# Optimization experiments

Measured on AMD Instinct MI355X. Metric: run time of the kernel, lower is better.

The kernel has to match this reference:

```python
import jax, jax.numpy as jnp
import numpy as np

KEY_IN = 256
QUERY_IN = 256
KEY_CH = 32
HEADS = 8
VAL_CH = 64
DK = KEY_CH // HEADS   # 4
DV = VAL_CH // HEADS   # 8
SCALE = DK ** -0.5


def _conv1x1(x, w, b):
    # x: [B,C,H,W], w: [O,C], b: [O] -> [B,O,H,W]
    return jnp.einsum('bchw,oc->bohw', x, w) + b[None, :, None, None]


def setup_inputs() -> dict:
    key = jax.random.key(0)
    ks = jax.random.split(key, 10)
    B, H, W = 8, 128, 128
    target = jax.random.normal(ks[0], (B, QUERY_IN, H, W), dtype=jnp.float32)
    inp = jax.random.normal(ks[1], (B, KEY_IN, H, W), dtype=jnp.float32)
    s = 0.02
    return {
        'target': target,
        'input': inp,
        'kw': jax.random.normal(ks[2], (KEY_CH, KEY_IN), dtype=jnp.float32) * s,
        'kb': jnp.zeros((KEY_CH,), dtype=jnp.float32),
        'qw': jax.random.normal(ks[3], (KEY_CH, QUERY_IN), dtype=jnp.float32) * s,
        'qb': jnp.zeros((KEY_CH,), dtype=jnp.float32),
        'vw': jax.random.normal(ks[4], (VAL_CH, KEY_IN), dtype=jnp.float32) * s,
        'vb': jnp.zeros((VAL_CH,), dtype=jnp.float32),
        'rw': jax.random.normal(ks[5], (QUERY_IN, VAL_CH), dtype=jnp.float32) * s,
        'rb': jnp.zeros((QUERY_IN,), dtype=jnp.float32),
    }


def reference(target, input, kw, kb, qw, qb, vw, vb, rw, rb):
    B, _, H, W = input.shape
    HW = H * W
    k = _conv1x1(input, kw, kb).reshape(B, HEADS, DK, HW)
    q = _conv1x1(target, qw, qb).reshape(B, HEADS, DK, HW)
    v = _conv1x1(input, vw, vb).reshape(B, HEADS, DV, HW)
    k = jax.nn.softmax(k, axis=-1)            # softmax over spatial positions
    q = jax.nn.softmax(q * SCALE, axis=-2)    # softmax over key-channel dim
    context = jnp.einsum('bhdn,bhen->bhde', k, v)   # [B,H,DK,DV]
    out = jnp.einsum('bhde,bhdn->bhen', context, q) # [B,H,DV,HW]
    out = out.reshape(B, VAL_CH, H, W)
    return _conv1x1(out, rw, rb)
```

## Files before the change

### kernel.cpp

```cpp
#include <hip/hip_runtime.h>
#include <hip/hip_bf16.h>
#include <math.h>

#define BATCH 8
#define HW 16384
#define CIN 256
#define KCH 32
#define VCH 64
#define HEADS 8
#define DK 4
#define DV 8
#define SCALE 0.5f

typedef _Float16 f16;
typedef f16 f16x8 __attribute__((ext_vector_type(8)));
typedef float f32x4 __attribute__((ext_vector_type(4)));

#define WS_WKVF 0
#define WS_QWF  12288
#define WS_RWF  16384
#define WS_KP   24576
#define WS_VP   (WS_KP + BATCH*16*HW)
#define WS_PART (WS_VP + BATCH*32*HW)
#define WS_CTX  (WS_PART + BATCH*HEADS*16*40)

__device__ inline unsigned pack_bf16(float a, float b) {
    unsigned ua = __float_as_uint(a);
    unsigned ub = __float_as_uint(b);
    ua = (ua + 0x7fffu + ((ua >> 16) & 1u)) >> 16;
    ub = (ub + 0x7fffu + ((ub >> 16) & 1u)) >> 16;
    return ua | (ub << 16);
}
__device__ inline float2 unpack_bf16(unsigned u) {
    float2 r;
    r.x = __uint_as_float(u << 16);
    r.y = __uint_as_float(u & 0xffff0000u);
    return r;
}
__device__ inline unsigned pk_f16(float a, float b) {
    auto h = __builtin_amdgcn_cvt_pkrtz(a, b);
    union { decltype(h) v; unsigned u; } c;
    c.v = h;
    return c.u;
}

#define GLDS16(g, l) __builtin_amdgcn_global_load_lds( \
    (__attribute__((address_space(1))) const void*)(g), \
    (__attribute__((address_space(3))) void*)(l), 16, 0, 0)

__global__ void prepack(const float* __restrict__ kw, const float* __restrict__ vw,
                        const float* __restrict__ qw, const float* __restrict__ rw,
                        f16* __restrict__ wkvf, f16* __restrict__ qwf, f16* __restrict__ rwf) {
    int t = blockIdx.x * 256 + threadIdx.x;
    int stride = gridDim.x * 256;
    for (int i = t; i < 6*8*64*8; i += stride) {
        int j = i & 7, lane = (i >> 3) & 63, kc = (i >> 9) & 7, mt = i >> 12;
        int row = mt*16 + (lane & 15);
        int k = kc*32 + (lane >> 4)*8 + j;
        float v = row < 32 ? kw[row*CIN + k] : vw[(row-32)*CIN + k];
        wkvf[i] = (f16)v;
    }
    for (int i = t; i < 2*8*64*8; i += stride) {
        int j = i & 7, lane = (i >> 3) & 63, kc = (i >> 9) & 7, mt = i >> 12;
        int row = mt*16 + (lane & 15);
        int k = kc*32 + (lane >> 4)*8 + j;
        qwf[i] = (f16)qw[row*CIN + k];
    }
    for (int i = t; i < 16*2*64*8; i += stride) {
        int j = i & 7, lane = (i >> 3) & 63, kc2 = (i >> 9) & 1, mt = i >> 10;
        int row = mt*16 + (lane & 15);
        int e = kc2*32 + (lane >> 4)*8 + j;
        rwf[i] = (f16)rw[row*VCH + e];
    }
}

__global__ void __launch_bounds__(256) proj_kv_mfma(const float* __restrict__ x,
    const f16* __restrict__ wkvf, const float* __restrict__ kb_,
    const float* __restrict__ vb_, unsigned* __restrict__ kp_out,
    unsigned* __restrict__ vp_out) {
    int b    = blockIdx.x >> 7;
    int bpx  = (blockIdx.x & 127) * 128;
    int wave = threadIdx.x >> 6, lane = threadIdx.x & 63;
    int wm = wave >> 1, wn = wave & 1;
    int col = lane & 15, kb = lane >> 4;
    int px0 = bpx + wn * 64;
    const float* Xb = x + (size_t)b * CIN * HW;

    f32x4 acc[3][4];
#pragma unroll
    for (int m = 0; m < 3; ++m)
#pragma unroll
        for (int n = 0; n < 4; ++n) acc[m][n] = (f32x4){0.f, 0.f, 0.f, 0.f};

    for (int kc = 0; kc < 8; ++kc) {
        f16x8 afr[3];
#pragma unroll
        for (int mt = 0; mt < 3; ++mt)
            afr[mt] = *(const f16x8*)(wkvf + (size_t)(((wm*3 + mt)*8 + kc)*64 + lane)*8);
        float xb[4][8];
#pragma unroll
        for (int nt = 0; nt < 4; ++nt)
#pragma unroll
            for (int j = 0; j < 8; ++j)
                xb[nt][j] = Xb[(size_t)(kc*32 + kb*8 + j)*HW + px0 + nt*16 + col];
        f16x8 bfr[4];
#pragma unroll
        for (int nt = 0; nt < 4; ++nt) {
            union { f16x8 v; unsigned u[4]; } u;
#pragma unroll
            for (int p = 0; p < 4; ++p)
                u.u[p] = pk_f16(xb[nt][2*p], xb[nt][2*p+1]);
            bfr[nt] = u.v;
        }
#pragma unroll
        for (int mt = 0; mt < 3; ++mt)
#pragma unroll
            for (int nt = 0; nt < 4; ++nt)
                acc[mt][nt] = __builtin_amdgcn_mfma_f32_16x16x32_f16(
                    afr[mt], bfr[nt], acc[mt][nt], 0, 0, 0);
    }

#pragma unroll
    for (int mt = 0; mt < 3; ++mt) {
        int row0 = wm*48 + mt*16 + kb*4;
        bool isk = row0 < 32;
        float4 bias = isk ? *(const float4*)(kb_ + row0)
                          : *(const float4*)(vb_ + row0 - 32);
#pragma unroll
        for (int nt = 0; nt < 4; ++nt) {
            int px = px0 + nt*16 + col;
            float v0 = acc[mt][nt][0] + bias.x;
            float v1 = acc[mt][nt][1] + bias.y;
            float v2 = acc[mt][nt][2] + bias.z;
            float v3 = acc[mt][nt][3] + bias.w;
            if (isk) {
                unsigned* kp = kp_out + (size_t)(b*16 + (row0 >> 1))*HW + px;
                kp[0]  = pack_bf16(expf(v0), expf(v1));
                kp[HW] = pack_bf16(expf(v2), expf(v3));
            } else {
                int vr = row0 - 32;
                unsigned* vp = vp_out + (size_t)(b*32 + (vr >> 1))*HW + px;
                vp[0]  = pack_bf16(v0, v1);
                vp[HW] = pack_bf16(v2, v3);
            }
        }
    }
}

__global__ void __launch_bounds__(256) ctx_partial(const unsigned* __restrict__ kp_in,
                                                   const unsigned* __restrict__ vp_in,
                                                   float* __restrict__ part) {
    int blk = blockIdx.x;
    int b  = blk >> 7;
    int h  = (blk >> 4) & 7;
    int ch = blk & 15;
    const unsigned* kp = kp_in + (size_t)b * 16 * HW + (size_t)(2*h) * HW;
    const unsigned* vp = vp_in + (size_t)b * 32 * HW + (size_t)(4*h) * HW;

    float den[DK] = {0.f, 0.f, 0.f, 0.f};
    float num[DK][DV] = {};

    int n0 = ch * 1024 + threadIdx.x;
#pragma unroll
    for (int it = 0; it < 4; ++it) {
        int n = n0 + it * 256;
        unsigned ku0 = kp[n], ku1 = kp[HW + n];
        unsigned vu0 = vp[n], vu1 = vp[HW + n];
        unsigned vu2 = vp[2*HW + n], vu3 = vp[3*HW + n];
        float2 k01 = unpack_bf16(ku0), k23 = unpack_bf16(ku1);
        float ek[DK] = {k01.x, k01.y, k23.x, k23.y};
        float2 va = unpack_bf16(vu0), vb2 = unpack_bf16(vu1);
        float2 vc = unpack_bf16(vu2), vd = unpack_bf16(vu3);
        float vv[DV] = {va.x, va.y, vb2.x, vb2.y, vc.x, vc.y, vd.x, vd.y};
#pragma unroll
        for (int d = 0; d < DK; ++d) {
            den[d] += ek[d];
#pragma unroll
            for (int e = 0; e < DV; ++e) num[d][e] += ek[d] * vv[e];
        }
    }

    __shared__ float red[36][4];
    int lane = threadIdx.x & 63;
    int wv   = threadIdx.x >> 6;
#pragma unroll
    for (int i = 0; i < 36; ++i) {
        float val = (i < 4) ? den[i] : num[(i - 4) >> 3][(i - 4) & 7];
        for (int off = 32; off; off >>= 1) val += __shfl_down(val, off);
        if (lane == 0) red[i][wv] = val;
    }
    __syncthreads();
    if (threadIdx.x < 36) {
        float s = red[threadIdx.x][0] + red[threadIdx.x][1] +
                  red[threadIdx.x][2] + red[threadIdx.x][3];
        part[(size_t)blk * 40 + threadIdx.x] = s;
    }
}

__global__ void ctx_final(const float* __restrict__ part,
                          float* __restrict__ ctx) {
    int b = blockIdx.x;
    int t = threadIdx.x;
    int h = t >> 5, d = (t >> 3) & 3, e = t & 7;
    float num = 0.f, den = 0.f;
#pragma unroll
    for (int ch = 0; ch < 16; ++ch) {
        const float* pp = part + (size_t)(((b * 8 + h) * 16 + ch)) * 40;
        num += pp[4 + d * 8 + e];
        den += pp[d];
    }
    ctx[(((size_t)b * 8 + h) * 8 + e) * 4 + d] = num / den;
}

#define FNT 2
__global__ void __launch_bounds__(256) fused_mfma(const float* __restrict__ tgt,
    const f16* __restrict__ qwf, const float* __restrict__ qb_,
    const float* __restrict__ ctx, const f16* __restrict__ rwf,
    const float* __restrict__ rb_, float* __restrict__ out) {
    __shared__ float tile[2][4096];
    int b    = blockIdx.x >> 7;
    int pxb  = (blockIdx.x & 127) * 128;
    int wave = threadIdx.x >> 6, lane = threadIdx.x & 63;
    int col = lane & 15, kb = lane >> 4;
    const float* Tb = tgt + (size_t)b * CIN * HW;

    int c0   = wave*8 + (lane >> 5);
    int px_g = pxb + (lane & 31)*4;

#pragma unroll
    for (int i = 0; i < 4; ++i)
        GLDS16(Tb + (size_t)(c0 + i*2)*HW + px_g, &tile[0][wave*1024 + i*256]);

    f32x4 qacc[2][FNT];
#pragma unroll
    for (int m = 0; m < 2; ++m)
#pragma unroll
        for (int n = 0; n < FNT; ++n) qacc[m][n] = (f32x4){0.f, 0.f, 0.f, 0.f};

    for (int kc = 0; kc < 8; ++kc) {
        int cur = kc & 1;
        __syncthreads();
        if (kc < 7) {
#pragma unroll
            for (int i = 0; i < 4; ++i)
                GLDS16(Tb + (size_t)((kc+1)*32 + c0 + i*2)*HW + px_g,
                       &tile[cur ^ 1][wave*1024 + i*256]);
        }
        f16x8 afr[2];
#pragma unroll
        for (int mt = 0; mt < 2; ++mt)
            afr[mt] = *(const f16x8*)(qwf + (size_t)((mt*8 + kc)*64 + lane)*8);
        f16x8 bfr[FNT];
#pragma unroll
        for (int nt = 0; nt < FNT; ++nt) {
            const float* tp = &tile[cur][kb*1024 + wave*32 + nt*16 + col];
            float x[8];
#pragma unroll
            for (int j = 0; j < 8; ++j) x[j] = tp[j*128];
            union { f16x8 v; unsigned u[4]; } u;
#pragma unroll
            for (int p = 0; p < 4; ++p)
                u.u[p] = pk_f16(x[2*p], x[2*p+1]);
            bfr[nt] = u.v;
        }
#pragma unroll
        for (int mt = 0; mt < 2; ++mt)
#pragma unroll
            for (int nt = 0; nt < FNT; ++nt)
                qacc[mt][nt] = __builtin_amdgcn_mfma_f32_16x16x32_f16(
                    afr[mt], bfr[nt], qacc[mt][nt], 0, 0, 0);
        __syncthreads();
    }

    unsigned attnu[2][FNT][4];
#pragma unroll
    for (int mt2 = 0; mt2 < 2; ++mt2) {
        int h = mt2*4 + kb;
        float4 qb4 = *(const float4*)(qb_ + mt2*16 + kb*4);
        float4 cx[8];
#pragma unroll
        for (int e = 0; e < 8; ++e)
            cx[e] = *(const float4*)(ctx + (size_t)((b*8 + h)*8 + e)*4);
#pragma unroll
        for (int nt = 0; nt < FNT; ++nt) {
            float s0 = (qacc[mt2][nt][0] + qb4.x) * SCALE;
            float s1 = (qacc[mt2][nt][1] + qb4.y) * SCALE;
            float s2 = (qacc[mt2][nt][2] + qb4.z) * SCALE;
            float s3 = (qacc[mt2][nt][3] + qb4.w) * SCALE;
            float m  = fmaxf(fmaxf(s0, s1), fmaxf(s2, s3));
            float e0 = expf(s0 - m), e1 = expf(s1 - m);
            float e2 = expf(s2 - m), e3 = expf(s3 - m);
            float inv = 1.f / (e0 + e1 + e2 + e3);
            float w0 = e0*inv, w1 = e1*inv, w2 = e2*inv, w3 = e3*inv;
            float at[8];
#pragma unroll
            for (int e = 0; e < 8; ++e)
                at[e] = cx[e].x*w0 + cx[e].y*w1 + cx[e].z*w2 + cx[e].w*w3;
#pragma unroll
            for (int p = 0; p < 4; ++p)
                attnu[mt2][nt][p] = pk_f16(at[2*p], at[2*p+1]);
        }
    }

    float* Ob = out + (size_t)b * CIN * HW;
    for (int pm = 0; pm < 4; ++pm) {
        f32x4 oacc[FNT][4];
#pragma unroll
        for (int n = 0; n < FNT; ++n)
#pragma unroll
            for (int m = 0; m < 4; ++m) oacc[n][m] = (f32x4){0.f, 0.f, 0.f, 0.f};
#pragma unroll
        for (int kc2 = 0; kc2 < 2; ++kc2) {
            f16x8 afr2[FNT];
#pragma unroll
            for (int nt = 0; nt < FNT; ++nt) {
                union { f16x8 v; unsigned u[4]; } c;
#pragma unroll
                for (int p = 0; p < 4; ++p) c.u[p] = attnu[kc2][nt][p];
                afr2[nt] = c.v;
            }
#pragma unroll
            for (int ot = 0; ot < 4; ++ot) {
                f16x8 bfr2 = *(const f16x8*)(rwf +
                    (size_t)((((pm*4 + ot)*2 + kc2)*64 + lane))*8);
#pragma unroll
                for (int nt = 0; nt < FNT; ++nt)
                    oacc[nt][ot] = __builtin_amdgcn_mfma_f32_16x16x32_f16(
                        afr2[nt], bfr2, oacc[nt][ot], 0, 0, 0);
            }
        }
#pragma unroll
        for (int ot = 0; ot < 4; ++ot) {
            int o = (pm*4 + ot)*16 + col;
            float rbv = rb_[o];
#pragma unroll
            for (int nt = 0; nt < FNT; ++nt) {
                int px = pxb + wave*32 + nt*16 + kb*4;
                float4 st = { oacc[nt][ot][0] + rbv, oacc[nt][ot][1] + rbv,
                              oacc[nt][ot][2] + rbv, oacc[nt][ot][3] + rbv };
                *(float4*)(Ob + (size_t)o * HW + px) = st;
            }
        }
    }
}

extern "C" void kernel_launch(void* const* d_in, const int* in_sizes, int n_in,
                              void* d_out, int out_size, void* d_ws, size_t ws_size,
                              hipStream_t stream) {
    const float* target = (const float*)d_in[0];
    const float* input  = (const float*)d_in[1];
    const float* kw = (const float*)d_in[2];
    const float* kb = (const float*)d_in[3];
    const float* qw = (const float*)d_in[4];
    const float* qb = (const float*)d_in[5];
    const float* vw = (const float*)d_in[6];
    const float* vb = (const float*)d_in[7];
    const float* rw = (const float*)d_in[8];
    const float* rb = (const float*)d_in[9];
    float* out = (float*)d_out;
    float* ws  = (float*)d_ws;

    f16*      wkvf = (f16*)(ws + WS_WKVF);
    f16*      qwf  = (f16*)(ws + WS_QWF);
    f16*      rwf  = (f16*)(ws + WS_RWF);
    unsigned* kp   = (unsigned*)(ws + WS_KP);
    unsigned* vp   = (unsigned*)(ws + WS_VP);
    float*    part = ws + WS_PART;
    float*    ctx  = ws + WS_CTX;

    hipLaunchKernelGGL(prepack, dim3(32), dim3(256), 0, stream,
                       kw, vw, qw, rw, wkvf, qwf, rwf);
    hipLaunchKernelGGL(proj_kv_mfma, dim3(BATCH * HW / 128), dim3(256), 0, stream,
                       input, wkvf, kb, vb, kp, vp);
    hipLaunchKernelGGL(ctx_partial, dim3(BATCH * HEADS * 16), dim3(256), 0, stream,
                       kp, vp, part);
    hipLaunchKernelGGL(ctx_final, dim3(BATCH), dim3(256), 0, stream,
                       part, ctx);
    hipLaunchKernelGGL(fused_mfma, dim3(BATCH * HW / 128), dim3(256), 0, stream,
                       target, qwf, qb, ctx, rwf, rb, out);
}
```

Measured before the change: 130.2 us.

## Split fused query/output kernel into separate q_attn and out_conv kernels

```diff
diff --git a/kernel.cpp b/kernel.cpp
--- a/kernel.cpp
+++ b/kernel.cpp
@@ -23,6 +23,7 @@
 #define WS_VP   (WS_KP + BATCH*16*HW)
 #define WS_PART (WS_VP + BATCH*32*HW)
 #define WS_CTX  (WS_PART + BATCH*HEADS*16*40)
+#define WS_ATT  (WS_CTX + BATCH*HEADS*DV*DK)
 
 __device__ inline unsigned pack_bf16(float a, float b) {
     unsigned ua = __float_as_uint(a);
@@ -43,10 +44,6 @@
     c.v = h;
     return c.u;
 }
-
-#define GLDS16(g, l) __builtin_amdgcn_global_load_lds( \
-    (__attribute__((address_space(1))) const void*)(g), \
-    (__attribute__((address_space(3))) void*)(l), 16, 0, 0)
 
 __global__ void prepack(const float* __restrict__ kw, const float* __restrict__ vw,
                         const float* __restrict__ qw, const float* __restrict__ rw,
@@ -213,24 +210,16 @@
 }
 
 #define FNT 2
-__global__ void __launch_bounds__(256) fused_mfma(const float* __restrict__ tgt,
+__global__ void __launch_bounds__(256) q_attn(const float* __restrict__ tgt,
     const f16* __restrict__ qwf, const float* __restrict__ qb_,
-    const float* __restrict__ ctx, const f16* __restrict__ rwf,
-    const float* __restrict__ rb_, float* __restrict__ out) {
-    __shared__ float tile[2][4096];
+    const float* __restrict__ ctx, uint4* __restrict__ att) {
     int b    = blockIdx.x >> 7;
     int pxb  = (blockIdx.x & 127) * 128;
     int wave = threadIdx.x >> 6, lane = threadIdx.x & 63;
     int col = lane & 15, kb = lane >> 4;
+    int px0 = pxb + wave * (FNT * 16);
     const float* Tb = tgt + (size_t)b * CIN * HW;
 
-    int c0   = wave*8 + (lane >> 5);
-    int px_g = pxb + (lane & 31)*4;
-
-#pragma unroll
-    for (int i = 0; i < 4; ++i)
-        GLDS16(Tb + (size_t)(c0 + i*2)*HW + px_g, &tile[0][wave*1024 + i*256]);
-
     f32x4 qacc[2][FNT];
 #pragma unroll
     for (int m = 0; m < 2; ++m)
@@ -238,29 +227,23 @@
         for (int n = 0; n < FNT; ++n) qacc[m][n] = (f32x4){0.f, 0.f, 0.f, 0.f};
 
     for (int kc = 0; kc < 8; ++kc) {
-        int cur = kc & 1;
-        __syncthreads();
-        if (kc < 7) {
-#pragma unroll
-            for (int i = 0; i < 4; ++i)
-                GLDS16(Tb + (size_t)((kc+1)*32 + c0 + i*2)*HW + px_g,
-                       &tile[cur ^ 1][wave*1024 + i*256]);
-        }
         f16x8 afr[2];
 #pragma unroll
         for (int mt = 0; mt < 2; ++mt)
             afr[mt] = *(const f16x8*)(qwf + (size_t)((mt*8 + kc)*64 + lane)*8);
+        float xb[FNT][8];
+#pragma unroll
+        for (int nt = 0; nt < FNT; ++nt)
+#pragma unroll
+            for (int j = 0; j < 8; ++j)
+                xb[nt][j] = Tb[(size_t)(kc*32 + kb*8 + j)*HW + px0 + nt*16 + col];
         f16x8 bfr[FNT];
 #pragma unroll
         for (int nt = 0; nt < FNT; ++nt) {
-            const float* tp = &tile[cur][kb*1024 + wave*32 + nt*16 + col];
-            float x[8];
-#pragma unroll
-            for (int j = 0; j < 8; ++j) x[j] = tp[j*128];
             union { f16x8 v; unsigned u[4]; } u;
 #pragma unroll
             for (int p = 0; p < 4; ++p)
-                u.u[p] = pk_f16(x[2*p], x[2*p+1]);
+                u.u[p] = pk_f16(xb[nt][2*p], xb[nt][2*p+1]);
             bfr[nt] = u.v;
         }
 #pragma unroll
@@ -269,10 +252,9 @@
             for (int nt = 0; nt < FNT; ++nt)
                 qacc[mt][nt] = __builtin_amdgcn_mfma_f32_16x16x32_f16(
                     afr[mt], bfr[nt], qacc[mt][nt], 0, 0, 0);
-        __syncthreads();
-    }
-
-    unsigned attnu[2][FNT][4];
+    }
+
+    uint4* ap = att + (size_t)blockIdx.x * 4 * 4 * 64;
 #pragma unroll
     for (int mt2 = 0; mt2 < 2; ++mt2) {
         int h = mt2*4 + kb;
@@ -296,11 +278,31 @@
 #pragma unroll
             for (int e = 0; e < 8; ++e)
                 at[e] = cx[e].x*w0 + cx[e].y*w1 + cx[e].z*w2 + cx[e].w*w3;
-#pragma unroll
-            for (int p = 0; p < 4; ++p)
-                attnu[mt2][nt][p] = pk_f16(at[2*p], at[2*p+1]);
-        }
-    }
+            uint4 st = { pk_f16(at[0], at[1]), pk_f16(at[2], at[3]),
+                         pk_f16(at[4], at[5]), pk_f16(at[6], at[7]) };
+            ap[(size_t)((wave*4 + mt2*2 + nt)*64) + lane] = st;
+        }
+    }
+}
+
+__global__ void __launch_bounds__(256) out_conv(const uint4* __restrict__ att,
+    const f16* __restrict__ rwf, const float* __restrict__ rb_,
+    float* __restrict__ out) {
+    int b    = blockIdx.x >> 7;
+    int pxb  = (blockIdx.x & 127) * 128;
+    int wave = threadIdx.x >> 6, lane = threadIdx.x & 63;
+    int col = lane & 15, kb = lane >> 4;
+    const uint4* ap = att + (size_t)blockIdx.x * 4 * 4 * 64 + wave*4*64 + lane;
+
+    f16x8 afr2[2][FNT];
+#pragma unroll
+    for (int kc2 = 0; kc2 < 2; ++kc2)
+#pragma unroll
+        for (int nt = 0; nt < FNT; ++nt) {
+            union { f16x8 v; uint4 q; } c;
+            c.q = ap[(kc2*2 + nt)*64];
+            afr2[kc2][nt] = c.v;
+        }
 
     float* Ob = out + (size_t)b * CIN * HW;
     for (int pm = 0; pm < 4; ++pm) {
@@ -311,14 +313,6 @@
             for (int m = 0; m < 4; ++m) oacc[n][m] = (f32x4){0.f, 0.f, 0.f, 0.f};
 #pragma unroll
         for (int kc2 = 0; kc2 < 2; ++kc2) {
-            f16x8 afr2[FNT];
-#pragma unroll
-            for (int nt = 0; nt < FNT; ++nt) {
-                union { f16x8 v; unsigned u[4]; } c;
-#pragma unroll
-                for (int p = 0; p < 4; ++p) c.u[p] = attnu[kc2][nt][p];
-                afr2[nt] = c.v;
-            }
 #pragma unroll
             for (int ot = 0; ot < 4; ++ot) {
                 f16x8 bfr2 = *(const f16x8*)(rwf +
@@ -326,7 +320,7 @@
 #pragma unroll
                 for (int nt = 0; nt < FNT; ++nt)
                     oacc[nt][ot] = __builtin_amdgcn_mfma_f32_16x16x32_f16(
-                        afr2[nt], bfr2, oacc[nt][ot], 0, 0, 0);
+                        afr2[kc2][nt], bfr2, oacc[nt][ot], 0, 0, 0);
             }
         }
 #pragma unroll
@@ -367,6 +361,7 @@
     unsigned* vp   = (unsigned*)(ws + WS_VP);
     float*    part = ws + WS_PART;
     float*    ctx  = ws + WS_CTX;
+    uint4*    att  = (uint4*)(ws + WS_ATT);
 
     hipLaunchKernelGGL(prepack, dim3(32), dim3(256), 0, stream,
                        kw, vw, qw, rw, wkvf, qwf, rwf);
@@ -376,6 +371,8 @@
                        kp, vp, part);
     hipLaunchKernelGGL(ctx_final, dim3(BATCH), dim3(256), 0, stream,
                        part, ctx);
-    hipLaunchKernelGGL(fused_mfma, dim3(BATCH * HW / 128), dim3(256), 0, stream,
-                       target, qwf, qb, ctx, rwf, rb, out);
-}
+    hipLaunchKernelGGL(q_attn, dim3(BATCH * HW / 128), dim3(256), 0, stream,
+                       target, qwf, qb, ctx, att);
+    hipLaunchKernelGGL(out_conv, dim3(BATCH * HW / 128), dim3(256), 0, stream,
+                       att, rwf, rb, out);
+}
```

Measured after the change: 132.0 us. No clear change (+1.4%).

## Fuse K/V projection with context partial reduction via LDS

Applied to the files above, without the earlier changes.

```diff
diff --git a/kernel.cpp b/kernel.cpp
--- a/kernel.cpp
+++ b/kernel.cpp
@@ -19,24 +19,9 @@
 #define WS_WKVF 0
 #define WS_QWF  12288
 #define WS_RWF  16384
-#define WS_KP   24576
-#define WS_VP   (WS_KP + BATCH*16*HW)
-#define WS_PART (WS_VP + BATCH*32*HW)
-#define WS_CTX  (WS_PART + BATCH*HEADS*16*40)
-
-__device__ inline unsigned pack_bf16(float a, float b) {
-    unsigned ua = __float_as_uint(a);
-    unsigned ub = __float_as_uint(b);
-    ua = (ua + 0x7fffu + ((ua >> 16) & 1u)) >> 16;
-    ub = (ub + 0x7fffu + ((ub >> 16) & 1u)) >> 16;
-    return ua | (ub << 16);
-}
-__device__ inline float2 unpack_bf16(unsigned u) {
-    float2 r;
-    r.x = __uint_as_float(u << 16);
-    r.y = __uint_as_float(u & 0xffff0000u);
-    return r;
-}
+#define WS_PART 24576
+#define WS_CTX  (WS_PART + BATCH*HEADS*128*40)
+
 __device__ inline unsigned pk_f16(float a, float b) {
     auto h = __builtin_amdgcn_cvt_pkrtz(a, b);
     union { decltype(h) v; unsigned u; } c;
@@ -74,12 +59,14 @@
     }
 }
 
-__global__ void __launch_bounds__(256) proj_kv_mfma(const float* __restrict__ x,
+__global__ void __launch_bounds__(256) proj_ctx(const float* __restrict__ x,
     const f16* __restrict__ wkvf, const float* __restrict__ kb_,
-    const float* __restrict__ vb_, unsigned* __restrict__ kp_out,
-    unsigned* __restrict__ vp_out) {
+    const float* __restrict__ vb_, float* __restrict__ part) {
+    __shared__ float ek_lds[KCH][129];
+    __shared__ float v_lds[VCH][129];
     int b    = blockIdx.x >> 7;
-    int bpx  = (blockIdx.x & 127) * 128;
+    int tile = blockIdx.x & 127;
+    int bpx  = tile * 128;
     int wave = threadIdx.x >> 6, lane = threadIdx.x & 63;
     int wm = wave >> 1, wn = wave & 1;
     int col = lane & 15, kb = lane >> 4;
@@ -128,72 +115,54 @@
                           : *(const float4*)(vb_ + row0 - 32);
 #pragma unroll
         for (int nt = 0; nt < 4; ++nt) {
-            int px = px0 + nt*16 + col;
+            int pxl = wn*64 + nt*16 + col;
             float v0 = acc[mt][nt][0] + bias.x;
             float v1 = acc[mt][nt][1] + bias.y;
             float v2 = acc[mt][nt][2] + bias.z;
             float v3 = acc[mt][nt][3] + bias.w;
             if (isk) {
-                unsigned* kp = kp_out + (size_t)(b*16 + (row0 >> 1))*HW + px;
-                kp[0]  = pack_bf16(expf(v0), expf(v1));
-                kp[HW] = pack_bf16(expf(v2), expf(v3));
+                ek_lds[row0+0][pxl] = expf(v0);
+                ek_lds[row0+1][pxl] = expf(v1);
+                ek_lds[row0+2][pxl] = expf(v2);
+                ek_lds[row0+3][pxl] = expf(v3);
             } else {
                 int vr = row0 - 32;
-                unsigned* vp = vp_out + (size_t)(b*32 + (vr >> 1))*HW + px;
-                vp[0]  = pack_bf16(v0, v1);
-                vp[HW] = pack_bf16(v2, v3);
-            }
-        }
-    }
-}
-
-__global__ void __launch_bounds__(256) ctx_partial(const unsigned* __restrict__ kp_in,
-                                                   const unsigned* __restrict__ vp_in,
-                                                   float* __restrict__ part) {
-    int blk = blockIdx.x;
-    int b  = blk >> 7;
-    int h  = (blk >> 4) & 7;
-    int ch = blk & 15;
-    const unsigned* kp = kp_in + (size_t)b * 16 * HW + (size_t)(2*h) * HW;
-    const unsigned* vp = vp_in + (size_t)b * 32 * HW + (size_t)(4*h) * HW;
-
-    float den[DK] = {0.f, 0.f, 0.f, 0.f};
-    float num[DK][DV] = {};
-
-    int n0 = ch * 1024 + threadIdx.x;
-#pragma unroll
-    for (int it = 0; it < 4; ++it) {
-        int n = n0 + it * 256;
-        unsigned ku0 = kp[n], ku1 = kp[HW + n];
-        unsigned vu0 = vp[n], vu1 = vp[HW + n];
-        unsigned vu2 = vp[2*HW + n], vu3 = vp[3*HW + n];
-        float2 k01 = unpack_bf16(ku0), k23 = unpack_bf16(ku1);
-        float ek[DK] = {k01.x, k01.y, k23.x, k23.y};
-        float2 va = unpack_bf16(vu0), vb2 = unpack_bf16(vu1);
-        float2 vc = unpack_bf16(vu2), vd = unpack_bf16(vu3);
-        float vv[DV] = {va.x, va.y, vb2.x, vb2.y, vc.x, vc.y, vd.x, vd.y};
-#pragma unroll
-        for (int d = 0; d < DK; ++d) {
-            den[d] += ek[d];
-#pragma unroll
-            for (int e = 0; e < DV; ++e) num[d][e] += ek[d] * vv[e];
-        }
-    }
-
-    __shared__ float red[36][4];
-    int lane = threadIdx.x & 63;
-    int wv   = threadIdx.x >> 6;
-#pragma unroll
-    for (int i = 0; i < 36; ++i) {
-        float val = (i < 4) ? den[i] : num[(i - 4) >> 3][(i - 4) & 7];
-        for (int off = 32; off; off >>= 1) val += __shfl_down(val, off);
-        if (lane == 0) red[i][wv] = val;
+                v_lds[vr+0][pxl] = v0;
+                v_lds[vr+1][pxl] = v1;
+                v_lds[vr+2][pxl] = v2;
+                v_lds[vr+3][pxl] = v3;
+            }
+        }
     }
     __syncthreads();
-    if (threadIdx.x < 36) {
-        float s = red[threadIdx.x][0] + red[threadIdx.x][1] +
-                  red[threadIdx.x][2] + red[threadIdx.x][3];
-        part[(size_t)blk * 40 + threadIdx.x] = s;
+
+#pragma unroll
+    for (int hh = 0; hh < 2; ++hh) {
+        int h = wave*2 + hh;
+        float den[DK] = {0.f, 0.f, 0.f, 0.f};
+        float num[DK][DV] = {};
+#pragma unroll
+        for (int pp = 0; pp < 2; ++pp) {
+            int px = lane + pp*64;
+            float ek[DK], vv[DV];
+#pragma unroll
+            for (int d = 0; d < DK; ++d) ek[d] = ek_lds[h*4 + d][px];
+#pragma unroll
+            for (int e = 0; e < DV; ++e) vv[e] = v_lds[h*8 + e][px];
+#pragma unroll
+            for (int d = 0; d < DK; ++d) {
+                den[d] += ek[d];
+#pragma unroll
+                for (int e = 0; e < DV; ++e) num[d][e] += ek[d] * vv[e];
+            }
+        }
+        float* pp_out = part + (size_t)(((b*8 + h)*128 + tile)) * 40;
+#pragma unroll
+        for (int j = 0; j < 36; ++j) {
+            float val = (j < 4) ? den[j] : num[(j - 4) >> 3][(j - 4) & 7];
+            for (int off = 32; off; off >>= 1) val += __shfl_down(val, off);
+            if (lane == 0) pp_out[j] = val;
+        }
     }
 }
 
@@ -203,9 +172,8 @@
     int t = threadIdx.x;
     int h = t >> 5, d = (t >> 3) & 3, e = t & 7;
     float num = 0.f, den = 0.f;
-#pragma unroll
-    for (int ch = 0; ch < 16; ++ch) {
-        const float* pp = part + (size_t)(((b * 8 + h) * 16 + ch)) * 40;
+    for (int ch = 0; ch < 128; ++ch) {
+        const float* pp = part + (size_t)(((b * 8 + h) * 128 + ch)) * 40;
         num += pp[4 + d * 8 + e];
         den += pp[d];
     }
@@ -254,13 +222,13 @@
 #pragma unroll
         for (int nt = 0; nt < FNT; ++nt) {
             const float* tp = &tile[cur][kb*1024 + wave*32 + nt*16 + col];
-            float x[8];
-#pragma unroll
-            for (int j = 0; j < 8; ++j) x[j] = tp[j*128];
+            float xv[8];
+#pragma unroll
+            for (int j = 0; j < 8; ++j) xv[j] = tp[j*128];
             union { f16x8 v; unsigned u[4]; } u;
 #pragma unroll
             for (int p = 0; p < 4; ++p)
-                u.u[p] = pk_f16(x[2*p], x[2*p+1]);
+                u.u[p] = pk_f16(xv[2*p], xv[2*p+1]);
             bfr[nt] = u.v;
         }
 #pragma unroll
@@ -360,20 +328,16 @@
     float* out = (float*)d_out;
     float* ws  = (float*)d_ws;
 
-    f16*      wkvf = (f16*)(ws + WS_WKVF);
-    f16*      qwf  = (f16*)(ws + WS_QWF);
-    f16*      rwf  = (f16*)(ws + WS_RWF);
-    unsigned* kp   = (unsigned*)(ws + WS_KP);
-    unsigned* vp   = (unsigned*)(ws + WS_VP);
-    float*    part = ws + WS_PART;
-    float*    ctx  = ws + WS_CTX;
+    f16*   wkvf = (f16*)(ws + WS_WKVF);
+    f16*   qwf  = (f16*)(ws + WS_QWF);
+    f16*   rwf  = (f16*)(ws + WS_RWF);
+    float* part = ws + WS_PART;
+    float* ctx  = ws + WS_CTX;
 
     hipLaunchKernelGGL(prepack, dim3(32), dim3(256), 0, stream,
                        kw, vw, qw, rw, wkvf, qwf, rwf);
-    hipLaunchKernelGGL(proj_kv_mfma, dim3(BATCH * HW / 128), dim3(256), 0, stream,
-                       input, wkvf, kb, vb, kp, vp);
-    hipLaunchKernelGGL(ctx_partial, dim3(BATCH * HEADS * 16), dim3(256), 0, stream,
-                       kp, vp, part);
+    hipLaunchKernelGGL(proj_ctx, dim3(BATCH * HW / 128), dim3(256), 0, stream,
+                       input, wkvf, kb, vb, part);
     hipLaunchKernelGGL(ctx_final, dim3(BATCH), dim3(256), 0, stream,
                        part, ctx);
     hipLaunchKernelGGL(fused_mfma, dim3(BATCH * HW / 128), dim3(256), 0, stream,
```

After: 149.8 us. 1.15x slower.

## Process four pixel tiles per block and drop LDS staging in fused kernel

Applied to the files above, without the earlier changes.

```diff
diff --git a/kernel.cpp b/kernel.cpp
--- a/kernel.cpp
+++ b/kernel.cpp
@@ -22,7 +22,7 @@
 #define WS_KP   24576
 #define WS_VP   (WS_KP + BATCH*16*HW)
 #define WS_PART (WS_VP + BATCH*32*HW)
-#define WS_CTX  (WS_PART + BATCH*HEADS*16*40)
+#define WS_CTX  (WS_PART + 1024*40)
 
 __device__ inline unsigned pack_bf16(float a, float b) {
     unsigned ua = __float_as_uint(a);
@@ -43,10 +43,6 @@
     c.v = h;
     return c.u;
 }
-
-#define GLDS16(g, l) __builtin_amdgcn_global_load_lds( \
-    (__attribute__((address_space(1))) const void*)(g), \
-    (__attribute__((address_space(3))) void*)(l), 16, 0, 0)
 
 __global__ void prepack(const float* __restrict__ kw, const float* __restrict__ vw,
                         const float* __restrict__ qw, const float* __restrict__ rw,
@@ -78,70 +74,73 @@
     const f16* __restrict__ wkvf, const float* __restrict__ kb_,
     const float* __restrict__ vb_, unsigned* __restrict__ kp_out,
     unsigned* __restrict__ vp_out) {
-    int b    = blockIdx.x >> 7;
-    int bpx  = (blockIdx.x & 127) * 128;
+    int b    = blockIdx.x >> 5;
+    int base = (blockIdx.x & 31) * 512;
     int wave = threadIdx.x >> 6, lane = threadIdx.x & 63;
     int wm = wave >> 1, wn = wave & 1;
     int col = lane & 15, kb = lane >> 4;
-    int px0 = bpx + wn * 64;
     const float* Xb = x + (size_t)b * CIN * HW;
 
-    f32x4 acc[3][4];
-#pragma unroll
-    for (int m = 0; m < 3; ++m)
-#pragma unroll
-        for (int n = 0; n < 4; ++n) acc[m][n] = (f32x4){0.f, 0.f, 0.f, 0.f};
-
-    for (int kc = 0; kc < 8; ++kc) {
-        f16x8 afr[3];
-#pragma unroll
-        for (int mt = 0; mt < 3; ++mt)
-            afr[mt] = *(const f16x8*)(wkvf + (size_t)(((wm*3 + mt)*8 + kc)*64 + lane)*8);
-        float xb[4][8];
-#pragma unroll
-        for (int nt = 0; nt < 4; ++nt)
-#pragma unroll
-            for (int j = 0; j < 8; ++j)
-                xb[nt][j] = Xb[(size_t)(kc*32 + kb*8 + j)*HW + px0 + nt*16 + col];
-        f16x8 bfr[4];
-#pragma unroll
-        for (int nt = 0; nt < 4; ++nt) {
-            union { f16x8 v; unsigned u[4]; } u;
-#pragma unroll
-            for (int p = 0; p < 4; ++p)
-                u.u[p] = pk_f16(xb[nt][2*p], xb[nt][2*p+1]);
-            bfr[nt] = u.v;
-        }
-#pragma unroll
-        for (int mt = 0; mt < 3; ++mt)
+    for (int st = 0; st < 4; ++st) {
+        int px0 = base + st*128 + wn * 64;
+
+        f32x4 acc[3][4];
+#pragma unroll
+        for (int m = 0; m < 3; ++m)
+#pragma unroll
+            for (int n = 0; n < 4; ++n) acc[m][n] = (f32x4){0.f, 0.f, 0.f, 0.f};
+
+        for (int kc = 0; kc < 8; ++kc) {
+            f16x8 afr[3];
+#pragma unroll
+            for (int mt = 0; mt < 3; ++mt)
+                afr[mt] = *(const f16x8*)(wkvf + (size_t)(((wm*3 + mt)*8 + kc)*64 + lane)*8);
+            float xb[4][8];
 #pragma unroll
             for (int nt = 0; nt < 4; ++nt)
-                acc[mt][nt] = __builtin_amdgcn_mfma_f32_16x16x32_f16(
-                    afr[mt], bfr[nt], acc[mt][nt], 0, 0, 0);
-    }
-
-#pragma unroll
-    for (int mt = 0; mt < 3; ++mt) {
-        int row0 = wm*48 + mt*16 + kb*4;
-        bool isk = row0 < 32;
-        float4 bias = isk ? *(const float4*)(kb_ + row0)
-                          : *(const float4*)(vb_ + row0 - 32);
-#pragma unroll
-        for (int nt = 0; nt < 4; ++nt) {
-            int px = px0 + nt*16 + col;
-            float v0 = acc[mt][nt][0] + bias.x;
-            float v1 = acc[mt][nt][1] + bias.y;
-            float v2 = acc[mt][nt][2] + bias.z;
-            float v3 = acc[mt][nt][3] + bias.w;
-            if (isk) {
-                unsigned* kp = kp_out + (size_t)(b*16 + (row0 >> 1))*HW + px;
-                kp[0]  = pack_bf16(expf(v0), expf(v1));
-                kp[HW] = pack_bf16(expf(v2), expf(v3));
-            } else {
-                int vr = row0 - 32;
-                unsigned* vp = vp_out + (size_t)(b*32 + (vr >> 1))*HW + px;
-                vp[0]  = pack_bf16(v0, v1);
-                vp[HW] = pack_bf16(v2, v3);
+#pragma unroll
+                for (int jj = 0; jj < 8; ++jj)
+                    xb[nt][jj] = Xb[(size_t)(kc*32 + kb*8 + jj)*HW + px0 + nt*16 + col];
+            f16x8 bfr[4];
+#pragma unroll
+            for (int nt = 0; nt < 4; ++nt) {
+                union { f16x8 v; unsigned u[4]; } u;
+#pragma unroll
+                for (int p = 0; p < 4; ++p)
+                    u.u[p] = pk_f16(xb[nt][2*p], xb[nt][2*p+1]);
+                bfr[nt] = u.v;
+            }
+#pragma unroll
+            for (int mt = 0; mt < 3; ++mt)
+#pragma unroll
+                for (int nt = 0; nt < 4; ++nt)
+                    acc[mt][nt] = __builtin_amdgcn_mfma_f32_16x16x32_f16(
+                        afr[mt], bfr[nt], acc[mt][nt], 0, 0, 0);
+        }
+
+#pragma unroll
+        for (int mt = 0; mt < 3; ++mt) {
+            int row0 = wm*48 + mt*16 + kb*4;
+            bool isk = row0 < 32;
+            float4 bias = isk ? *(const float4*)(kb_ + row0)
+                              : *(const float4*)(vb_ + row0 - 32);
+#pragma unroll
+            for (int nt = 0; nt < 4; ++nt) {
+                int px = px0 + nt*16 + col;
+                float v0 = acc[mt][nt][0] + bias.x;
+                float v1 = acc[mt][nt][1] + bias.y;
+                float v2 = acc[mt][nt][2] + bias.z;
+                float v3 = acc[mt][nt][3] + bias.w;
+                if (isk) {
+                    unsigned* kp = kp_out + (size_t)(b*16 + (row0 >> 1))*HW + px;
+                    kp[0]  = pack_bf16(expf(v0), expf(v1));
+                    kp[HW] = pack_bf16(expf(v2), expf(v3));
+                } else {
+                    int vr = row0 - 32;
+                    unsigned* vp = vp_out + (size_t)(b*32 + (vr >> 1))*HW + px;
+                    vp[0]  = pack_bf16(v0, v1);
+                    vp[HW] = pack_bf16(v2, v3);
+                }
             }
         }
     }
@@ -159,7 +158,6 @@
 
     float den[DK] = {0.f, 0.f, 0.f, 0.f};
     float num[DK][DV] = {};
-
     int n0 = ch * 1024 + threadIdx.x;
 #pragma unroll
     for (int it = 0; it < 4; ++it) {
@@ -179,7 +177,6 @@
             for (int e = 0; e < DV; ++e) num[d][e] += ek[d] * vv[e];
         }
     }
-
     __shared__ float red[36][4];
     int lane = threadIdx.x & 63;
     int wv   = threadIdx.x >> 6;
@@ -197,8 +194,7 @@
     }
 }
 
-__global__ void ctx_final(const float* __restrict__ part,
-                          float* __restrict__ ctx) {
+__global__ void ctx_final(const float* __restrict__ part, float* __restrict__ ctx) {
     int b = blockIdx.x;
     int t = threadIdx.x;
     int h = t >> 5, d = (t >> 3) & 3, e = t & 7;
@@ -217,128 +213,124 @@
     const f16* __restrict__ qwf, const float* __restrict__ qb_,
     const float* __restrict__ ctx, const f16* __restrict__ rwf,
     const float* __restrict__ rb_, float* __restrict__ out) {
-    __shared__ float tile[2][4096];
-    int b    = blockIdx.x >> 7;
-    int pxb  = (blockIdx.x & 127) * 128;
+    int b    = blockIdx.x >> 5;
+    int base = (blockIdx.x & 31) * 512;
     int wave = threadIdx.x >> 6, lane = threadIdx.x & 63;
     int col = lane & 15, kb = lane >> 4;
     const float* Tb = tgt + (size_t)b * CIN * HW;
-
-    int c0   = wave*8 + (lane >> 5);
-    int px_g = pxb + (lane & 31)*4;
-
-#pragma unroll
-    for (int i = 0; i < 4; ++i)
-        GLDS16(Tb + (size_t)(c0 + i*2)*HW + px_g, &tile[0][wave*1024 + i*256]);
-
-    f32x4 qacc[2][FNT];
-#pragma unroll
-    for (int m = 0; m < 2; ++m)
-#pragma unroll
-        for (int n = 0; n < FNT; ++n) qacc[m][n] = (f32x4){0.f, 0.f, 0.f, 0.f};
-
-    for (int kc = 0; kc < 8; ++kc) {
-        int cur = kc & 1;
-        __syncthreads();
-        if (kc < 7) {
-#pragma unroll
-            for (int i = 0; i < 4; ++i)
-                GLDS16(Tb + (size_t)((kc+1)*32 + c0 + i*2)*HW + px_g,
-                       &tile[cur ^ 1][wave*1024 + i*256]);
-        }
-        f16x8 afr[2];
-#pragma unroll
-        for (int mt = 0; mt < 2; ++mt)
-            afr[mt] = *(const f16x8*)(qwf + (size_t)((mt*8 + kc)*64 + lane)*8);
-        f16x8 bfr[FNT];
-#pragma unroll
-        for (int nt = 0; nt < FNT; ++nt) {
-            const float* tp = &tile[cur][kb*1024 + wave*32 + nt*16 + col];
-            float x[8];
-#pragma unroll
-            for (int j = 0; j < 8; ++j) x[j] = tp[j*128];
-            union { f16x8 v; unsigned u[4]; } u;
-#pragma unroll
-            for (int p = 0; p < 4; ++p)
-                u.u[p] = pk_f16(x[2*p], x[2*p+1]);
-            bfr[nt] = u.v;
-        }
-#pragma unroll
-        for (int mt = 0; mt < 2; ++mt)
-#pragma unroll
-            for (int nt = 0; nt < FNT; ++nt)
-                qacc[mt][nt] = __builtin_amdgcn_mfma_f32_16x16x32_f16(
-                    afr[mt], bfr[nt], qacc[mt][nt], 0, 0, 0);
-        __syncthreads();
-    }
-
-    unsigned attnu[2][FNT][4];
+    float* Ob = out + (size_t)b * CIN * HW;
+
+    float4 cxa[2][8];
+    float4 qb4a[2];
 #pragma unroll
     for (int mt2 = 0; mt2 < 2; ++mt2) {
         int h = mt2*4 + kb;
-        float4 qb4 = *(const float4*)(qb_ + mt2*16 + kb*4);
-        float4 cx[8];
+        qb4a[mt2] = *(const float4*)(qb_ + mt2*16 + kb*4);
 #pragma unroll
         for (int e = 0; e < 8; ++e)
-            cx[e] = *(const float4*)(ctx + (size_t)((b*8 + h)*8 + e)*4);
-#pragma unroll
-        for (int nt = 0; nt < FNT; ++nt) {
-            float s0 = (qacc[mt2][nt][0] + qb4.x) * SCALE;
-            float s1 = (qacc[mt2][nt][1] + qb4.y) * SCALE;
-            float s2 = (qacc[mt2][nt][2] + qb4.z) * SCALE;
-            float s3 = (qacc[mt2][nt][3] + qb4.w) * SCALE;
-            float m  = fmaxf(fmaxf(s0, s1), fmaxf(s2, s3));
-            float e0 = expf(s0 - m), e1 = expf(s1 - m);
-            float e2 = expf(s2 - m), e3 = expf(s3 - m);
-            float inv = 1.f / (e0 + e1 + e2 + e3);
-            float w0 = e0*inv, w1 = e1*inv, w2 = e2*inv, w3 = e3*inv;
-            float at[8];
-#pragma unroll
-            for (int e = 0; e < 8; ++e)
-                at[e] = cx[e].x*w0 + cx[e].y*w1 + cx[e].z*w2 + cx[e].w*w3;
-#pragma unroll
-            for (int p = 0; p < 4; ++p)
-                attnu[mt2][nt][p] = pk_f16(at[2*p], at[2*p+1]);
-        }
-    }
-
-    float* Ob = out + (size_t)b * CIN * HW;
-    for (int pm = 0; pm < 4; ++pm) {
-        f32x4 oacc[FNT][4];
-#pragma unroll
-        for (int n = 0; n < FNT; ++n)
-#pragma unroll
-            for (int m = 0; m < 4; ++m) oacc[n][m] = (f32x4){0.f, 0.f, 0.f, 0.f};
-#pragma unroll
-        for (int kc2 = 0; kc2 < 2; ++kc2) {
-            f16x8 afr2[FNT];
+            cxa[mt2][e] = *(const float4*)(ctx + (size_t)((b*8 + h)*8 + e)*4);
+    }
+
+    for (int st = 0; st < 4; ++st) {
+        int px0 = base + st*128 + wave * (FNT * 16);
+
+        f32x4 qacc[2][FNT];
+#pragma unroll
+        for (int m = 0; m < 2; ++m)
+#pragma unroll
+            for (int n = 0; n < FNT; ++n) qacc[m][n] = (f32x4){0.f, 0.f, 0.f, 0.f};
+
+        for (int kc = 0; kc < 8; ++kc) {
+            f16x8 afr[2];
+#pragma unroll
+            for (int mt = 0; mt < 2; ++mt)
+                afr[mt] = *(const f16x8*)(qwf + (size_t)((mt*8 + kc)*64 + lane)*8);
+            float xb[FNT][8];
+#pragma unroll
+            for (int nt = 0; nt < FNT; ++nt)
+#pragma unroll
+                for (int jj = 0; jj < 8; ++jj)
+                    xb[nt][jj] = Tb[(size_t)(kc*32 + kb*8 + jj)*HW + px0 + nt*16 + col];
+            f16x8 bfr[FNT];
 #pragma unroll
             for (int nt = 0; nt < FNT; ++nt) {
-                union { f16x8 v; unsigned u[4]; } c;
-#pragma unroll
-                for (int p = 0; p < 4; ++p) c.u[p] = attnu[kc2][nt][p];
-                afr2[nt] = c.v;
+                union { f16x8 v; unsigned u[4]; } u;
+#pragma unroll
+                for (int p = 0; p < 4; ++p)
+                    u.u[p] = pk_f16(xb[nt][2*p], xb[nt][2*p+1]);
+                bfr[nt] = u.v;
+            }
+#pragma unroll
+            for (int mt = 0; mt < 2; ++mt)
+#pragma unroll
+                for (int nt = 0; nt < FNT; ++nt)
+                    qacc[mt][nt] = __builtin_amdgcn_mfma_f32_16x16x32_f16(
+                        afr[mt], bfr[nt], qacc[mt][nt], 0, 0, 0);
+        }
+
+        unsigned attnu[2][FNT][4];
+#pragma unroll
+        for (int mt2 = 0; mt2 < 2; ++mt2) {
+            float4 qb4 = qb4a[mt2];
+#pragma unroll
+            for (int nt = 0; nt < FNT; ++nt) {
+                float s0 = (qacc[mt2][nt][0] + qb4.x) * SCALE;
+                float s1 = (qacc[mt2][nt][1] + qb4.y) * SCALE;
+                float s2 = (qacc[mt2][nt][2] + qb4.z) * SCALE;
+                float s3 = (qacc[mt2][nt][3] + qb4.w) * SCALE;
+                float m  = fmaxf(fmaxf(s0, s1), fmaxf(s2, s3));
+                float e0 = expf(s0 - m), e1 = expf(s1 - m);
+                float e2 = expf(s2 - m), e3 = expf(s3 - m);
+                float inv = 1.f / (e0 + e1 + e2 + e3);
+                float w0 = e0*inv, w1 = e1*inv, w2 = e2*inv, w3 = e3*inv;
+                float at[8];
+#pragma unroll
+                for (int e = 0; e < 8; ++e)
+                    at[e] = cxa[mt2][e].x*w0 + cxa[mt2][e].y*w1
+                          + cxa[mt2][e].z*w2 + cxa[mt2][e].w*w3;
+#pragma unroll
+                for (int p = 0; p < 4; ++p)
+                    attnu[mt2][nt][p] = pk_f16(at[2*p], at[2*p+1]);
+            }
+        }
+
+        for (int pm = 0; pm < 4; ++pm) {
+            f32x4 oacc[FNT][4];
+#pragma unroll
+            for (int n = 0; n < FNT; ++n)
+#pragma unroll
+                for (int m = 0; m < 4; ++m) oacc[n][m] = (f32x4){0.f, 0.f, 0.f, 0.f};
+#pragma unroll
+            for (int kc2 = 0; kc2 < 2; ++kc2) {
+                f16x8 afr2[FNT];
+#pragma unroll
+                for (int nt = 0; nt < FNT; ++nt) {
+                    union { f16x8 v; unsigned u[4]; } c;
+#pragma unroll
+                    for (int p = 0; p < 4; ++p) c.u[p] = attnu[kc2][nt][p];
+                    afr2[nt] = c.v;
+                }
+#pragma unroll
+                for (int ot = 0; ot < 4; ++ot) {
+                    f16x8 bfr2 = *(const f16x8*)(rwf +
+                        (size_t)((((pm*4 + ot)*2 + kc2)*64 + lane))*8);
+#pragma unroll
+                    for (int nt = 0; nt < FNT; ++nt)
+                        oacc[nt][ot] = __builtin_amdgcn_mfma_f32_16x16x32_f16(
+                            afr2[nt], bfr2, oacc[nt][ot], 0, 0, 0);
+                }
             }
 #pragma unroll
             for (int ot = 0; ot < 4; ++ot) {
-                f16x8 bfr2 = *(const f16x8*)(rwf +
-                    (size_t)((((pm*4 + ot)*2 + kc2)*64 + lane))*8);
-#pragma unroll
-                for (int nt = 0; nt < FNT; ++nt)
-                    oacc[nt][ot] = __builtin_amdgcn_mfma_f32_16x16x32_f16(
-                        afr2[nt], bfr2, oacc[nt][ot], 0, 0, 0);
-            }
-        }
-#pragma unroll
-        for (int ot = 0; ot < 4; ++ot) {
-            int o = (pm*4 + ot)*16 + col;
-            float rbv = rb_[o];
-#pragma unroll
-            for (int nt = 0; nt < FNT; ++nt) {
-                int px = pxb + wave*32 + nt*16 + kb*4;
-                float4 st = { oacc[nt][ot][0] + rbv, oacc[nt][ot][1] + rbv,
-                              oacc[nt][ot][2] + rbv, oacc[nt][ot][3] + rbv };
-                *(float4*)(Ob + (size_t)o * HW + px) = st;
+                int o = (pm*4 + ot)*16 + col;
+                float rbv = rb_[o];
+#pragma unroll
+                for (int nt = 0; nt < FNT; ++nt) {
+                    int px = base + st*128 + wave*32 + nt*16 + kb*4;
+                    float4 stv = { oacc[nt][ot][0] + rbv, oacc[nt][ot][1] + rbv,
+                                   oacc[nt][ot][2] + rbv, oacc[nt][ot][3] + rbv };
+                    *(float4*)(Ob + (size_t)o * HW + px) = stv;
+                }
             }
         }
     }
@@ -370,12 +362,12 @@
 
     hipLaunchKernelGGL(prepack, dim3(32), dim3(256), 0, stream,
                        kw, vw, qw, rw, wkvf, qwf, rwf);
-    hipLaunchKernelGGL(proj_kv_mfma, dim3(BATCH * HW / 128), dim3(256), 0, stream,
+    hipLaunchKernelGGL(proj_kv_mfma, dim3(BATCH * HW / 512), dim3(256), 0, stream,
                        input, wkvf, kb, vb, kp, vp);
     hipLaunchKernelGGL(ctx_partial, dim3(BATCH * HEADS * 16), dim3(256), 0, stream,
                        kp, vp, part);
     hipLaunchKernelGGL(ctx_final, dim3(BATCH), dim3(256), 0, stream,
                        part, ctx);
-    hipLaunchKernelGGL(fused_mfma, dim3(BATCH * HW / 128), dim3(256), 0, stream,
+    hipLaunchKernelGGL(fused_mfma, dim3(BATCH * HW / 512), dim3(256), 0, stream,
                        target, qwf, qb, ctx, rwf, rb, out);
 }
```

After: 192.9 us. +48.1%, slower.
